# Performance work log

Measured on AMD Instinct MI355X. Metric: run time of the kernel, lower is better.

## Reference

```python
import jax, jax.numpy as jnp
import numpy as np

B, S, D = 2, 2048, 768
H, DK, F = 12, 64, 3072
LN_EPS = 1e-5


def setup_inputs() -> dict:
    key = jax.random.key(0)
    ks = jax.random.split(key, 8)
    w = lambda k, shape: jax.random.normal(k, shape, dtype=jnp.float32) * 0.02
    return {
        "x": jax.random.normal(ks[0], (B, S, D), dtype=jnp.float32),
        "wq_w": w(ks[1], (H, D, DK)), "wq_b": jnp.zeros((H, DK), jnp.float32),
        "wk_w": w(ks[2], (H, D, DK)), "wk_b": jnp.zeros((H, DK), jnp.float32),
        "wv_w": w(ks[3], (H, D, DK)), "wv_b": jnp.zeros((H, DK), jnp.float32),
        "wo_w": w(ks[4], (H * DK, D)), "wo_b": jnp.zeros((D,), jnp.float32),
        "ln_g": jnp.ones((D,), jnp.float32), "ln_b": jnp.zeros((D,), jnp.float32),
        "w1": w(ks[5], (D, F)), "b1": jnp.zeros((F,), jnp.float32),
        "w2": w(ks[6], (F, D)), "b2": jnp.zeros((D,), jnp.float32),
    }


def layer_norm(x, g, b):
    mu = jnp.mean(x, axis=-1, keepdims=True)
    var = jnp.mean(jnp.square(x - mu), axis=-1, keepdims=True)
    return (x - mu) * jax.lax.rsqrt(var + LN_EPS) * g + b


def reference(x, wq_w, wq_b, wk_w, wk_b, wv_w, wv_b, wo_w, wo_b,
              ln_g, ln_b, w1, b1, w2, b2):
    dk = wq_w.shape[-1]
    x_res = x
    h = layer_norm(x, ln_b=ln_b, g=ln_g, b=ln_b) if False else layer_norm(x, ln_g, ln_b)
    # per-head QKV (all heads batched via einsum): [B,H,S,DK]
    q = jnp.einsum("bsd,hdk->bhsk", h, wq_w) + wq_b[None, :, None, :]
    k = jnp.einsum("bsd,hdk->bhsk", h, wk_w) + wk_b[None, :, None, :]
    v = jnp.einsum("bsd,hdk->bhsk", h, wv_w) + wv_b[None, :, None, :]
    scores = jnp.einsum("bhqk,bhsk->bhqs", q, k) / jnp.sqrt(jnp.float32(dk))
    attn = jax.nn.softmax(scores, axis=-1)
    o = jnp.einsum("bhqs,bhsk->bhqk", attn, v)  # [B,H,S,DK]
    Bx, Hx, Sx, Dkx = o.shape
    o = o.transpose(0, 2, 1, 3).reshape(Bx, Sx, Hx * Dkx)  # concat heads
    y = o @ wo_w + wo_b + x_res  # residual 1
    y_res = y
    z = layer_norm(y, ln_g, ln_b)
    z = jax.nn.gelu(z @ w1 + b1, approximate=False) @ w2 + b2
    return z + y_res
```

## Files before the change

kernel.cpp:

```cpp
#include <hip/hip_runtime.h>
#include <hip/hip_bf16.h>
#include <math.h>

typedef __bf16 bf16_t;
typedef __bf16 bf16x8 __attribute__((ext_vector_type(8)));
typedef __bf16 bf16x4 __attribute__((ext_vector_type(4)));
typedef float f32x4 __attribute__((ext_vector_type(4)));

#define MFMA_B16(a, b, c) __builtin_amdgcn_mfma_f32_16x16x32_bf16((a), (b), (c), 0, 0, 0)

static constexpr int Bn = 2, Sn = 2048, Dn = 768, Hn = 12, Fn = 3072;
static constexpr int NTOK = Bn * Sn;
#define QSCALE 0.18033688011112042f

__device__ __forceinline__ void gl_lds16(const bf16_t* g, void* lds) {
  __builtin_amdgcn_global_load_lds(
      (const __attribute__((address_space(1))) uint32_t*)g,
      (__attribute__((address_space(3))) uint32_t*)lds, 16, 0, 0);
}

__global__ __launch_bounds__(256) void k_prep(const float* __restrict__ wq, const float* __restrict__ wk,
                                              const float* __restrict__ wv, const float* __restrict__ wo,
                                              const float* __restrict__ w1, const float* __restrict__ w2,
                                              const float* __restrict__ bq, const float* __restrict__ bk,
                                              const float* __restrict__ bv,
                                              bf16_t* __restrict__ WqkvT, bf16_t* __restrict__ WoT,
                                              bf16_t* __restrict__ W1T, bf16_t* __restrict__ W2T,
                                              float* __restrict__ QKVB) {
  int t = blockIdx.x;
  if (t >= 1728) {
    for (int i = threadIdx.x; i < 2304; i += 256)
      QKVB[i] = i < 768 ? bq[i] : (i < 1536 ? bk[i - 768] : bv[i - 1536]);
    return;
  }
  __shared__ float T[64][65];
  const float* src;
  bf16_t* dst;
  int P, Q, tp, tq;
  if (t < 432) {
    int pb = t / 12; tp = t - pb * 12; tq = 0;
    int proj = pb / 12, head = pb - proj * 12;
    src = (proj == 0 ? wq : proj == 1 ? wk : wv) + (size_t)head * 768 * 64;
    dst = WqkvT + (size_t)proj * 589824 + (size_t)head * 64 * 768;
    P = 768; Q = 64;
  } else if (t < 576) {
    int u = t - 432; tp = u / 12; tq = u - tp * 12;
    src = wo; dst = WoT; P = 768; Q = 768;
  } else if (t < 1152) {
    int u = t - 576; tp = u / 48; tq = u - tp * 48;
    src = w1; dst = W1T; P = 768; Q = 3072;
  } else {
    int u = t - 1152; tp = u / 12; tq = u - tp * 12;
    src = w2; dst = W2T; P = 3072; Q = 768;
  }
  int j = threadIdx.x & 63, i0 = threadIdx.x >> 6;
#pragma unroll
  for (int i = i0; i < 64; i += 4)
    T[i][j] = src[(size_t)(tp * 64 + i) * Q + tq * 64 + j];
  __syncthreads();
#pragma unroll
  for (int i = i0; i < 64; i += 4)
    dst[(size_t)(tq * 64 + i) * P + tp * 64 + j] = (bf16_t)T[j][i];
}

__global__ __launch_bounds__(256) void k_layernorm(const float* __restrict__ x,
                                                   const float* __restrict__ g,
                                                   const float* __restrict__ bb,
                                                   bf16_t* __restrict__ out) {
  int t = blockIdx.x, tid = threadIdx.x;
  const float* xr = x + (size_t)t * Dn;
  float v0 = xr[tid], v1 = xr[tid + 256], v2 = xr[tid + 512];
  float s = v0 + v1 + v2;
  float ss = v0 * v0 + v1 * v1 + v2 * v2;
  __shared__ float red[8];
#pragma unroll
  for (int off = 32; off > 0; off >>= 1) {
    s += __shfl_down(s, off);
    ss += __shfl_down(ss, off);
  }
  int w = tid >> 6, l = tid & 63;
  if (l == 0) { red[w] = s; red[4 + w] = ss; }
  __syncthreads();
  s = red[0] + red[1] + red[2] + red[3];
  ss = red[4] + red[5] + red[6] + red[7];
  float mu = s * (1.0f / Dn);
  float var = ss * (1.0f / Dn) - mu * mu;
  float rstd = rsqrtf(var + 1e-5f);
  bf16_t* orow = out + (size_t)t * Dn;
  orow[tid]       = (bf16_t)((v0 - mu) * rstd * g[tid]       + bb[tid]);
  orow[tid + 256] = (bf16_t)((v1 - mu) * rstd * g[tid + 256] + bb[tid + 256]);
  orow[tid + 512] = (bf16_t)((v2 - mu) * rstd * g[tid + 512] + bb[tid + 512]);
}

enum { EPI_QK = 0, EPI_VT = 1, EPI_Y = 2, EPI_GELU = 3, EPI_OUT = 4 };

template <int MT, int NT, int EPI, int OCC>
__global__ __launch_bounds__(256, OCC) void k_gemm(const bf16_t* __restrict__ A,
                                                   const bf16_t* __restrict__ Bt,
                                                   int N, int K,
                                                   const float* __restrict__ bias,
                                                   const float* __restrict__ resid,
                                                   void* __restrict__ out0,
                                                   void* __restrict__ out1) {
  constexpr int MI = MT / 32, NI = NT / 32;
  constexpr int WROWS = MT / 2, WCOLS = NT / 2;
  __shared__ __align__(16) bf16_t As[2][MT * 32];
  __shared__ __align__(16) bf16_t Bs[2][NT * 32];
  const int tid = threadIdx.x;
  const int w = tid >> 6, l = tid & 63;
  const int wm = w >> 1, wn = w & 1;
  const int mloc = l & 15, kblk = l >> 4;
  const int bx = blockIdx.x, by = blockIdx.y;

  f32x4 acc[MI][NI];
#pragma unroll
  for (int i = 0; i < MI; ++i)
#pragma unroll
    for (int j = 0; j < NI; ++j) acc[i][j] = f32x4{0.f, 0.f, 0.f, 0.f};

  const int r0 = tid >> 2, ko0 = (tid & 3) * 8;
  const bf16_t* gA = A + (size_t)(by * MT + r0) * K + ko0;
  const bf16_t* gB = Bt + (size_t)(bx * NT + r0) * K + ko0;
  const int nk = K >> 5;

  {
    char* lA = (char*)&As[0][0] + w * 1024;
    char* lB = (char*)&Bs[0][0] + w * 1024;
    gl_lds16(gA, lA);
    if constexpr (MT == 128) gl_lds16(gA + (size_t)64 * K, lA + 4096);
    gl_lds16(gB, lB);
    if constexpr (NT == 128) gl_lds16(gB + (size_t)64 * K, lB + 4096);
  }

  for (int kt = 0; kt < nk; ++kt) {
    __syncthreads();
    if (kt + 1 < nk) {
      const bf16_t* nA = gA + (size_t)(kt + 1) * 32;
      const bf16_t* nB = gB + (size_t)(kt + 1) * 32;
      char* lA = (char*)&As[(kt + 1) & 1][0] + w * 1024;
      char* lB = (char*)&Bs[(kt + 1) & 1][0] + w * 1024;
      gl_lds16(nA, lA);
      if constexpr (MT == 128) gl_lds16(nA + (size_t)64 * K, lA + 4096);
      gl_lds16(nB, lB);
      if constexpr (NT == 128) gl_lds16(nB + (size_t)64 * K, lB + 4096);
    }
    const bf16_t* Ab = &As[kt & 1][0];
    const bf16_t* Bb = &Bs[kt & 1][0];
    bf16x8 af[MI], bfv[NI];
#pragma unroll
    for (int mi = 0; mi < MI; ++mi)
      af[mi] = *(const bf16x8*)&Ab[(wm * WROWS + mi * 16 + mloc) * 32 + kblk * 8];
#pragma unroll
    for (int ni = 0; ni < NI; ++ni)
      bfv[ni] = *(const bf16x8*)&Bb[(wn * WCOLS + ni * 16 + mloc) * 32 + kblk * 8];
#pragma unroll
    for (int mi = 0; mi < MI; ++mi)
#pragma unroll
      for (int ni = 0; ni < NI; ++ni)
        acc[mi][ni] = MFMA_B16(af[mi], bfv[ni], acc[mi][ni]);
  }

  const int gmb = by * MT + wm * WROWS + kblk * 4;
  const int gnb = bx * NT + wn * WCOLS + mloc;
  if constexpr (EPI == EPI_QK) {
    const int proj = bx / 6;
#pragma unroll
    for (int mi = 0; mi < MI; ++mi)
#pragma unroll
      for (int ni = 0; ni < NI; ++ni) {
        int gn = gnb + ni * 16;
        float bv = bias[gn];
        int gm0 = gmb + mi * 16;
        if (proj == 0) {
          bf16_t* dst = (bf16_t*)out0;
#pragma unroll
          for (int r = 0; r < 4; ++r)
            dst[(size_t)(gm0 + r) * 768 + gn] = (bf16_t)((acc[mi][ni][r] + bv) * QSCALE);
        } else {
          bf16_t* dst = (bf16_t*)out1;
#pragma unroll
          for (int r = 0; r < 4; ++r)
            dst[(size_t)(gm0 + r) * 768 + (gn - 768)] = (bf16_t)(acc[mi][ni][r] + bv);
        }
      }
  } else if constexpr (EPI == EPI_VT) {
    bf16_t* dst = (bf16_t*)out0;
#pragma unroll
    for (int mi = 0; mi < MI; ++mi)
#pragma unroll
      for (int ni = 0; ni < NI; ++ni) {
        int gn = gnb + ni * 16;
        int bq = gn >> 11, sq = gn & 2047;
#pragma unroll
        for (int r = 0; r < 4; ++r) {
          int gm = gmb + mi * 16 + r;
          int hq = gm >> 6, dk = gm & 63;
          dst[((size_t)(bq * Hn + hq) * 64 + dk) * Sn + sq] = (bf16_t)(acc[mi][ni][r] + bias[gm]);
        }
      }
  } else if constexpr (EPI == EPI_GELU) {
    bf16_t* dst = (bf16_t*)out0;
#pragma unroll
    for (int mi = 0; mi < MI; ++mi)
#pragma unroll
      for (int ni = 0; ni < NI; ++ni) {
        int gn = gnb + ni * 16;
        float bv = bias[gn];
#pragma unroll
        for (int r = 0; r < 4; ++r) {
          int gm = gmb + mi * 16 + r;
          float t = acc[mi][ni][r] + bv;
          float ge = 0.5f * t * (1.0f + erff(t * 0.70710678118654752f));
          dst[(size_t)gm * N + gn] = (bf16_t)ge;
        }
      }
  } else {
    float* dst = (float*)out0;
#pragma unroll
    for (int mi = 0; mi < MI; ++mi)
#pragma unroll
      for (int ni = 0; ni < NI; ++ni) {
        int gn = gnb + ni * 16;
        float bv = bias[gn];
#pragma unroll
        for (int r = 0; r < 4; ++r) {
          int gm = gmb + mi * 16 + r;
          dst[(size_t)gm * N + gn] = acc[mi][ni][r] + bv + resid[(size_t)gm * N + gn];
        }
      }
  }
}

__global__ __launch_bounds__(256, 3) void k_attn(const bf16_t* __restrict__ Q,
                                                 const bf16_t* __restrict__ K,
                                                 const bf16_t* __restrict__ VT,
                                                 bf16_t* __restrict__ O) {
  __shared__ __align__(16) bf16_t Ks[2][2 * 64 * 32];
  __shared__ __align__(16) bf16_t Vs[2][2 * 64 * 32];
  const int tid = threadIdx.x, w = tid >> 6, l = tid & 63;
  const int mloc = l & 15, kblk = l >> 4;
  const int bh = blockIdx.y, b = bh / Hn, h = bh - b * Hn;
  const int q0 = blockIdx.x * 64;

  const size_t qoff = (size_t)(b * Sn + q0 + w * 16 + mloc) * Dn + h * 64 + kblk * 8;
  const bf16x8 qf0 = *(const bf16x8*)(Q + qoff);
  const bf16x8 qf1 = *(const bf16x8*)(Q + qoff + 32);

  bf16x8 ones;
#pragma unroll
  for (int j = 0; j < 8; ++j) ones[j] = (bf16_t)1.0f;

  const int row = tid >> 2, q4 = tid & 3;
  const int srow = (row & 0x23) | ((row & 0x0C) << 1) | ((row & 0x10) >> 2);
  const bf16_t* Kg = K + (size_t)(b * Sn + srow) * Dn + h * 64 + q4 * 8;
  const bf16_t* Vg = VT + ((size_t)bh * 64 + row) * Sn + q4 * 8;

  f32x4 lacc = f32x4{0.f, 0.f, 0.f, 0.f};
  f32x4 oacc[4];
#pragma unroll
  for (int md = 0; md < 4; ++md) oacc[md] = f32x4{0.f, 0.f, 0.f, 0.f};

  {
    char* lK = (char*)&Ks[0][0] + w * 1024;
    char* lV = (char*)&Vs[0][0] + w * 1024;
    gl_lds16(Kg, lK);
    gl_lds16(Kg + 32, lK + 4096);
    gl_lds16(Vg, lV);
    gl_lds16(Vg + 32, lV + 4096);
  }

  for (int it = 0; it < Sn / 64; ++it) {
    __syncthreads();
    if (it + 1 < Sn / 64) {
      const int kv1 = (it + 1) * 64;
      char* lK = (char*)&Ks[(it + 1) & 1][0] + w * 1024;
      char* lV = (char*)&Vs[(it + 1) & 1][0] + w * 1024;
      gl_lds16(Kg + (size_t)kv1 * Dn, lK);
      gl_lds16(Kg + (size_t)kv1 * Dn + 32, lK + 4096);
      gl_lds16(Vg + kv1, lV);
      gl_lds16(Vg + kv1 + 32, lV + 4096);
    }
    const bf16_t* Kb = &Ks[it & 1][0];
    const bf16_t* Vb = &Vs[it & 1][0];

    f32x4 st[4];
#pragma unroll
    for (int ns = 0; ns < 4; ++ns) {
      const bf16x8 k0 = *(const bf16x8*)&Kb[(ns * 16 + mloc) * 32 + kblk * 8];
      const bf16x8 k1 = *(const bf16x8*)&Kb[2048 + (ns * 16 + mloc) * 32 + kblk * 8];
      f32x4 a = f32x4{0.f, 0.f, 0.f, 0.f};
      a = MFMA_B16(k0, qf0, a);
      a = MFMA_B16(k1, qf1, a);
      st[ns] = a;
    }

    bf16x8 pb0, pb1;
#pragma unroll
    for (int j = 0; j < 4; ++j) {
      pb0[j]     = (bf16_t)__builtin_amdgcn_exp2f(st[0][j]);
      pb0[4 + j] = (bf16_t)__builtin_amdgcn_exp2f(st[1][j]);
      pb1[j]     = (bf16_t)__builtin_amdgcn_exp2f(st[2][j]);
      pb1[4 + j] = (bf16_t)__builtin_amdgcn_exp2f(st[3][j]);
    }

    lacc = MFMA_B16(ones, pb0, lacc);
    lacc = MFMA_B16(ones, pb1, lacc);

#pragma unroll
    for (int md = 0; md < 4; ++md) {
      const bf16x8 v0 = *(const bf16x8*)&Vb[(md * 16 + mloc) * 32 + kblk * 8];
      const bf16x8 v1 = *(const bf16x8*)&Vb[2048 + (md * 16 + mloc) * 32 + kblk * 8];
      oacc[md] = MFMA_B16(v0, pb0, oacc[md]);
      oacc[md] = MFMA_B16(v1, pb1, oacc[md]);
    }
  }

  const float inv = 1.0f / lacc[0];
  const size_t obase = (size_t)(b * Sn + q0 + w * 16 + mloc) * Dn + h * 64 + kblk * 4;
#pragma unroll
  for (int md = 0; md < 4; ++md) {
    bf16x4 o4;
#pragma unroll
    for (int r = 0; r < 4; ++r) o4[r] = (bf16_t)(oacc[md][r] * inv);
    *(bf16x4*)&O[obase + md * 16] = o4;
  }
}

extern "C" void kernel_launch(void* const* d_in, const int* in_sizes, int n_in,
                              void* d_out, int out_size, void* d_ws, size_t ws_size,
                              hipStream_t stream) {
  (void)in_sizes; (void)n_in; (void)out_size; (void)ws_size;
  const float* x    = (const float*)d_in[0];
  const float* wq_w = (const float*)d_in[1];
  const float* wq_b = (const float*)d_in[2];
  const float* wk_w = (const float*)d_in[3];
  const float* wk_b = (const float*)d_in[4];
  const float* wv_w = (const float*)d_in[5];
  const float* wv_b = (const float*)d_in[6];
  const float* wo_w = (const float*)d_in[7];
  const float* wo_b = (const float*)d_in[8];
  const float* ln_g = (const float*)d_in[9];
  const float* ln_b = (const float*)d_in[10];
  const float* w1   = (const float*)d_in[11];
  const float* b1   = (const float*)d_in[12];
  const float* w2   = (const float*)d_in[13];
  const float* b2   = (const float*)d_in[14];

  char* ws = (char*)d_ws;
  size_t o = 0;
  bf16_t* WqkvT = (bf16_t*)(ws + o); o += (size_t)2304 * 768 * 2;
  bf16_t* WoT   = (bf16_t*)(ws + o); o += (size_t)768 * 768 * 2;
  bf16_t* W1T   = (bf16_t*)(ws + o); o += (size_t)3072 * 768 * 2;
  bf16_t* W2T   = (bf16_t*)(ws + o); o += (size_t)768 * 3072 * 2;
  float*  QKVB  = (float*)(ws + o);  o += (size_t)2304 * 4;
  bf16_t* Hbuf  = (bf16_t*)(ws + o); o += (size_t)NTOK * 768 * 2;
  bf16_t* Qb    = (bf16_t*)(ws + o); o += (size_t)NTOK * 768 * 2;
  bf16_t* Kb    = (bf16_t*)(ws + o); o += (size_t)NTOK * 768 * 2;
  bf16_t* VbT   = (bf16_t*)(ws + o); o += (size_t)NTOK * 768 * 2;
  float*  Ybuf  = (float*)(ws + o);  o += (size_t)NTOK * 768 * 4;
  bf16_t* Zbuf  = (bf16_t*)(ws + o); o += (size_t)NTOK * 768 * 2;
  bf16_t* Ubuf  = (bf16_t*)(ws + o); o += (size_t)NTOK * 3072 * 2;

  k_prep<<<1729, 256, 0, stream>>>(wq_w, wk_w, wv_w, wo_w, w1, w2,
                                   wq_b, wk_b, wv_b, WqkvT, WoT, W1T, W2T, QKVB);

  k_layernorm<<<NTOK, 256, 0, stream>>>(x, ln_g, ln_b, Hbuf);

  k_gemm<64, 128, EPI_QK, 4><<<dim3(12, 64), 256, 0, stream>>>(Hbuf, WqkvT, 1536, 768,
                                                               QKVB, nullptr, Qb, Kb);

  k_gemm<64, 64, EPI_VT, 4><<<dim3(64, 12), 256, 0, stream>>>(WqkvT + (size_t)2 * 589824, Hbuf,
                                                              4096, 768, QKVB + 1536, nullptr,
                                                              VbT, nullptr);

  k_attn<<<dim3(Sn / 64, Bn * Hn), 256, 0, stream>>>(Qb, Kb, VbT, Hbuf);

  k_gemm<64, 64, EPI_Y, 4><<<dim3(12, 64), 256, 0, stream>>>(Hbuf, WoT, 768, 768,
                                                             wo_b, x, Ybuf, nullptr);

  k_layernorm<<<NTOK, 256, 0, stream>>>(Ybuf, ln_g, ln_b, Zbuf);

  k_gemm<128, 128, EPI_GELU, 3><<<dim3(24, 32), 256, 0, stream>>>(Zbuf, W1T, 3072, 768,
                                                                  b1, nullptr, Ubuf, nullptr);

  k_gemm<64, 64, EPI_OUT, 4><<<dim3(12, 64), 256, 0, stream>>>(Ubuf, W2T, 768, 3072,
                                                               b2, Ybuf, d_out, nullptr);
}
```

Before: 296.1 us.

## Register-staged multi-stage GEMM prefetch with padded LDS and XCD-aware block swizzle

Replaces direct global-to-LDS loads with register-staged loads that prefetch 2-3 k-tiles ahead. Tiles are written into LDS with a padded row stride of 40 to avoid bank conflicts on fragment reads, and the per-iteration barrier moves to after the next-tile store. It also adds an optional block-index remap that gives each XCD a contiguous band of M-tiles for L2 locality, and lowers the QK GEMM occupancy hint to 3. The extra staging registers raise register pressure, which may limit occupancy.

```diff
diff --git a/kernel.cpp b/kernel.cpp
--- a/kernel.cpp
+++ b/kernel.cpp
@@ -94,7 +94,7 @@
 
 enum { EPI_QK = 0, EPI_VT = 1, EPI_Y = 2, EPI_GELU = 3, EPI_OUT = 4 };
 
-template <int MT, int NT, int EPI, int OCC>
+template <int MT, int NT, int EPI, int OCC, int SWZ>
 __global__ __launch_bounds__(256, OCC) void k_gemm(const bf16_t* __restrict__ A,
                                                    const bf16_t* __restrict__ Bt,
                                                    int N, int K,
@@ -104,13 +104,22 @@
                                                    void* __restrict__ out1) {
   constexpr int MI = MT / 32, NI = NT / 32;
   constexpr int WROWS = MT / 2, WCOLS = NT / 2;
-  __shared__ __align__(16) bf16_t As[2][MT * 32];
-  __shared__ __align__(16) bf16_t Bs[2][NT * 32];
+  constexpr int CA = MT / 64, CB = NT / 64;
+  constexpr int PF = (MT == 128) ? 2 : 3;
+  constexpr int LDW = 40;
+  __shared__ __align__(16) bf16_t As[2][MT * LDW];
+  __shared__ __align__(16) bf16_t Bs[2][NT * LDW];
   const int tid = threadIdx.x;
   const int w = tid >> 6, l = tid & 63;
   const int wm = w >> 1, wn = w & 1;
   const int mloc = l & 15, kblk = l >> 4;
-  const int bx = blockIdx.x, by = blockIdx.y;
+  int bx = blockIdx.x, by = blockIdx.y;
+  if constexpr (SWZ) {
+    int lin = by * gridDim.x + bx;
+    int xcd = lin & 7, s = lin >> 3;
+    by = xcd * (gridDim.y >> 3) + s / gridDim.x;
+    bx = s - (s / gridDim.x) * gridDim.x;
+  }
 
   f32x4 acc[MI][NI];
 #pragma unroll
@@ -118,46 +127,58 @@
 #pragma unroll
     for (int j = 0; j < NI; ++j) acc[i][j] = f32x4{0.f, 0.f, 0.f, 0.f};
 
-  const int r0 = tid >> 2, ko0 = (tid & 3) * 8;
-  const bf16_t* gA = A + (size_t)(by * MT + r0) * K + ko0;
-  const bf16_t* gB = Bt + (size_t)(bx * NT + r0) * K + ko0;
+  const int rr = tid >> 2, gg = (tid & 3) * 8;
+  const bf16_t* gA = A + (size_t)(by * MT + rr) * K + gg;
+  const bf16_t* gB = Bt + (size_t)(bx * NT + rr) * K + gg;
+  const int lofs = rr * LDW + gg;
   const int nk = K >> 5;
 
-  {
-    char* lA = (char*)&As[0][0] + w * 1024;
-    char* lB = (char*)&Bs[0][0] + w * 1024;
-    gl_lds16(gA, lA);
-    if constexpr (MT == 128) gl_lds16(gA + (size_t)64 * K, lA + 4096);
-    gl_lds16(gB, lB);
-    if constexpr (NT == 128) gl_lds16(gB + (size_t)64 * K, lB + 4096);
-  }
-
+  uint4 stA[PF][CA], stB[PF][CB];
+#pragma unroll
+  for (int s = 0; s < PF; ++s) {
+#pragma unroll
+    for (int c = 0; c < CA; ++c) stA[s][c] = *(const uint4*)(gA + (size_t)c * 64 * K + s * 32);
+#pragma unroll
+    for (int c = 0; c < CB; ++c) stB[s][c] = *(const uint4*)(gB + (size_t)c * 64 * K + s * 32);
+  }
+#pragma unroll
+  for (int c = 0; c < CA; ++c) *(uint4*)&As[0][lofs + c * 64 * LDW] = stA[0][c];
+#pragma unroll
+  for (int c = 0; c < CB; ++c) *(uint4*)&Bs[0][lofs + c * 64 * LDW] = stB[0][c];
+  __syncthreads();
+
+  int p = 0;
+  int snext = 1 % PF;
+  int sload = 0;
   for (int kt = 0; kt < nk; ++kt) {
-    __syncthreads();
-    if (kt + 1 < nk) {
-      const bf16_t* nA = gA + (size_t)(kt + 1) * 32;
-      const bf16_t* nB = gB + (size_t)(kt + 1) * 32;
-      char* lA = (char*)&As[(kt + 1) & 1][0] + w * 1024;
-      char* lB = (char*)&Bs[(kt + 1) & 1][0] + w * 1024;
-      gl_lds16(nA, lA);
-      if constexpr (MT == 128) gl_lds16(nA + (size_t)64 * K, lA + 4096);
-      gl_lds16(nB, lB);
-      if constexpr (NT == 128) gl_lds16(nB + (size_t)64 * K, lB + 4096);
-    }
-    const bf16_t* Ab = &As[kt & 1][0];
-    const bf16_t* Bb = &Bs[kt & 1][0];
     bf16x8 af[MI], bfv[NI];
 #pragma unroll
     for (int mi = 0; mi < MI; ++mi)
-      af[mi] = *(const bf16x8*)&Ab[(wm * WROWS + mi * 16 + mloc) * 32 + kblk * 8];
+      af[mi] = *(const bf16x8*)&As[p][(wm * WROWS + mi * 16 + mloc) * LDW + kblk * 8];
 #pragma unroll
     for (int ni = 0; ni < NI; ++ni)
-      bfv[ni] = *(const bf16x8*)&Bb[(wn * WCOLS + ni * 16 + mloc) * 32 + kblk * 8];
+      bfv[ni] = *(const bf16x8*)&Bs[p][(wn * WCOLS + ni * 16 + mloc) * LDW + kblk * 8];
+    if (kt + PF < nk) {
+#pragma unroll
+      for (int c = 0; c < CA; ++c) stA[sload][c] = *(const uint4*)(gA + (size_t)c * 64 * K + (kt + PF) * 32);
+#pragma unroll
+      for (int c = 0; c < CB; ++c) stB[sload][c] = *(const uint4*)(gB + (size_t)c * 64 * K + (kt + PF) * 32);
+    }
 #pragma unroll
     for (int mi = 0; mi < MI; ++mi)
 #pragma unroll
       for (int ni = 0; ni < NI; ++ni)
         acc[mi][ni] = MFMA_B16(af[mi], bfv[ni], acc[mi][ni]);
+    if (kt + 1 < nk) {
+#pragma unroll
+      for (int c = 0; c < CA; ++c) *(uint4*)&As[p ^ 1][lofs + c * 64 * LDW] = stA[snext][c];
+#pragma unroll
+      for (int c = 0; c < CB; ++c) *(uint4*)&Bs[p ^ 1][lofs + c * 64 * LDW] = stB[snext][c];
+      __syncthreads();
+    }
+    p ^= 1;
+    sload = snext;
+    snext = (snext + 1 == PF) ? 0 : snext + 1;
   }
 
   const int gmb = by * MT + wm * WROWS + kblk * 4;
@@ -366,23 +387,23 @@
 
   k_layernorm<<<NTOK, 256, 0, stream>>>(x, ln_g, ln_b, Hbuf);
 
-  k_gemm<64, 128, EPI_QK, 4><<<dim3(12, 64), 256, 0, stream>>>(Hbuf, WqkvT, 1536, 768,
-                                                               QKVB, nullptr, Qb, Kb);
-
-  k_gemm<64, 64, EPI_VT, 4><<<dim3(64, 12), 256, 0, stream>>>(WqkvT + (size_t)2 * 589824, Hbuf,
-                                                              4096, 768, QKVB + 1536, nullptr,
-                                                              VbT, nullptr);
+  k_gemm<64, 128, EPI_QK, 3, 1><<<dim3(12, 64), 256, 0, stream>>>(Hbuf, WqkvT, 1536, 768,
+                                                                  QKVB, nullptr, Qb, Kb);
+
+  k_gemm<64, 64, EPI_VT, 4, 0><<<dim3(64, 12), 256, 0, stream>>>(WqkvT + (size_t)2 * 589824, Hbuf,
+                                                                 4096, 768, QKVB + 1536, nullptr,
+                                                                 VbT, nullptr);
 
   k_attn<<<dim3(Sn / 64, Bn * Hn), 256, 0, stream>>>(Qb, Kb, VbT, Hbuf);
 
-  k_gemm<64, 64, EPI_Y, 4><<<dim3(12, 64), 256, 0, stream>>>(Hbuf, WoT, 768, 768,
-                                                             wo_b, x, Ybuf, nullptr);
+  k_gemm<64, 64, EPI_Y, 4, 1><<<dim3(12, 64), 256, 0, stream>>>(Hbuf, WoT, 768, 768,
+                                                                wo_b, x, Ybuf, nullptr);
 
   k_layernorm<<<NTOK, 256, 0, stream>>>(Ybuf, ln_g, ln_b, Zbuf);
 
-  k_gemm<128, 128, EPI_GELU, 3><<<dim3(24, 32), 256, 0, stream>>>(Zbuf, W1T, 3072, 768,
-                                                                  b1, nullptr, Ubuf, nullptr);
-
-  k_gemm<64, 64, EPI_OUT, 4><<<dim3(12, 64), 256, 0, stream>>>(Ubuf, W2T, 768, 3072,
-                                                               b2, Ybuf, d_out, nullptr);
-}
+  k_gemm<128, 128, EPI_GELU, 3, 1><<<dim3(24, 32), 256, 0, stream>>>(Zbuf, W1T, 3072, 768,
+                                                                     b1, nullptr, Ubuf, nullptr);
+
+  k_gemm<64, 64, EPI_OUT, 4, 1><<<dim3(12, 64), 256, 0, stream>>>(Ubuf, W2T, 768, 3072,
+                                                                  b2, Ybuf, d_out, nullptr);
+}
```

New measurement: 585.0 us. 1.98x slower.
